# Performance work log

Measured on AMD Instinct MI355X. Metric: run time of the kernel, lower is better.

The kernel has to match this reference:

```python
import jax, jax.numpy as jnp
import numpy as np

B, T, D, H = 4, 2048, 1024, 16
HD = D // H          # head_size = 64
FF = 16 * D          # FeedForward hidden = 16*n_embd per source
EPS = 1e-5


def layer_norm(x, g, b):
    mu = jnp.mean(x, axis=-1, keepdims=True)
    var = jnp.mean(jnp.square(x - mu), axis=-1, keepdims=True)
    return (x - mu) * jax.lax.rsqrt(var + EPS) * g + b


def setup_inputs() -> dict:
    key = jax.random.key(0)
    ks = jax.random.split(key, 17)
    s_d = 1.0 / np.sqrt(D)
    s_ff = 1.0 / np.sqrt(FF)
    return {
        "x": jax.random.normal(ks[0], (B, T, D), jnp.float32),
        # per-head Q/K/V linears, batched over heads: [H, D, HD]
        "Wq": jax.random.normal(ks[1], (H, D, HD), jnp.float32) * s_d,
        "bq": jax.random.normal(ks[2], (H, HD), jnp.float32) * s_d,
        "Wk": jax.random.normal(ks[3], (H, D, HD), jnp.float32) * s_d,
        "bk": jax.random.normal(ks[4], (H, HD), jnp.float32) * s_d,
        "Wv": jax.random.normal(ks[5], (H, D, HD), jnp.float32) * s_d,
        "bv": jax.random.normal(ks[6], (H, HD), jnp.float32) * s_d,
        "Wo": jax.random.normal(ks[7], (D, D), jnp.float32) * s_d,
        "bo": jax.random.normal(ks[8], (D,), jnp.float32) * s_d,
        "ln1_g": jnp.ones((D,), jnp.float32),
        "ln1_b": jnp.zeros((D,), jnp.float32),
        "W1": jax.random.normal(ks[9], (D, FF), jnp.float32) * s_d,
        "b1": jax.random.normal(ks[10], (FF,), jnp.float32) * s_d,
        "W2": jax.random.normal(ks[11], (FF, D), jnp.float32) * s_ff,
        "b2": jax.random.normal(ks[12], (D,), jnp.float32) * s_ff,
        "ln2_g": jnp.ones((D,), jnp.float32),
        "ln2_b": jnp.zeros((D,), jnp.float32),
    }


def reference(x, Wq, bq, Wk, bk, Wv, bv, Wo, bo, ln1_g, ln1_b,
              W1, b1, W2, b2, ln2_g, ln2_b):
    # --- multi-head causal self-attention (all heads batched) ---
    q = jnp.einsum('btd,hdk->bhtk', x, Wq) + bq[None, :, None, :]
    k = jnp.einsum('btd,hdk->bhtk', x, Wk) + bk[None, :, None, :]
    v = jnp.einsum('btd,hdk->bhtk', x, Wv) + bv[None, :, None, :]
    scores = jnp.einsum('bhtk,bhsk->bhts', q, k) / np.sqrt(HD)
    causal = jnp.tril(jnp.ones((T, T), bool))
    scores = jnp.where(causal, scores, -jnp.inf)
    attn = jax.nn.softmax(scores, axis=-1)
    out = jnp.einsum('bhts,bhsk->bhtk', attn, v)
    out = out.transpose(0, 2, 1, 3).reshape(x.shape[0], x.shape[1], H * HD)
    attn_out = out @ Wo + bo
    # --- post-LN residual structure, as in the source ---
    out1 = layer_norm(x + attn_out, ln1_g, ln1_b)
    ff = jax.nn.relu(out1 @ W1 + b1) @ W2 + b2
    out2 = layer_norm(out1 + ff, ln2_g, ln2_b)
    return out2
```

## Files before the change

### kernel.cpp

```cpp
#include <hip/hip_runtime.h>

typedef unsigned short u16;
typedef unsigned int   u32;
typedef __attribute__((ext_vector_type(8))) short short8;
typedef __attribute__((ext_vector_type(4))) float f32x4;

#define DEV static __device__ __forceinline__

DEV u16 f2bf(float x) {
  union { float f; u32 u; } c; c.f = x;
  u32 r = c.u + 0x7fffu + ((c.u >> 16) & 1u);
  return (u16)(r >> 16);
}

struct __align__(8) us4 { u16 a, b, c, d; };

DEV void gload16(const void* g, void* l) {
  __builtin_amdgcn_global_load_lds(
      (const __attribute__((address_space(1))) void*)g,
      (__attribute__((address_space(3))) void*)l, 16, 0, 0);
}

template<int EPI>
__global__ __launch_bounds__(256)
void gemm_bt(const u16* __restrict__ A, const u16* __restrict__ Bt,
             const float* __restrict__ bias, const float* __restrict__ resid,
             float* __restrict__ outf, u16* __restrict__ outb,
             u16* __restrict__ q_out, u16* __restrict__ k_out, u16* __restrict__ vt_out,
             int M, int N, int K)
{
  __shared__ __align__(16) u16 As[128 * 64];
  __shared__ __align__(16) u16 Bs[128 * 64];
  const int tid = threadIdx.x;
  const int lane = tid & 63;
  const int wave = tid >> 6;
  const int wm = wave >> 1, wn = wave & 1;
  const int lo = lane & 15, hi = lane >> 4;

  const int nwg = gridDim.x * gridDim.y;
  int bid = blockIdx.y * gridDim.x + blockIdx.x;
  bid = (bid & 7) * (nwg >> 3) + (bid >> 3);
  const int bm = (bid / gridDim.x) * 128;
  const int bn = (bid % gridDim.x) * 128;

  const int kchunk = K / gridDim.z;
  const int kbeg = blockIdx.z * kchunk;
  const int kend = kbeg + kchunk;

  f32x4 zero = {0.f, 0.f, 0.f, 0.f};
  f32x4 acc[4][4];
#pragma unroll
  for (int i = 0; i < 4; ++i)
#pragma unroll
    for (int j = 0; j < 4; ++j) acc[i][j] = zero;

  for (int k0 = kbeg; k0 < kend; k0 += 64) {
#pragma unroll
    for (int i = 0; i < 4; ++i) {
      int slot = i * 4096 + tid * 16;
      int row  = slot >> 7;
      int c16  = (slot >> 4) & 7;
      int gc   = (c16 ^ (row & 7)) * 8;
      gload16(A  + (size_t)(bm + row) * K + k0 + gc,
              (char*)As + i * 4096 + wave * 1024);
      gload16(Bt + (size_t)(bn + row) * K + k0 + gc,
              (char*)Bs + i * 4096 + wave * 1024);
    }
    __syncthreads();
#pragma unroll
    for (int kk = 0; kk < 2; ++kk) {
      short8 a[4], b[4];
      int ks = kk * 4 + hi;
#pragma unroll
      for (int mi = 0; mi < 4; ++mi) {
        int row = wm * 64 + mi * 16 + lo;
        a[mi] = *(const short8*)&As[row * 64 + ((ks ^ (row & 7)) * 8)];
      }
#pragma unroll
      for (int ni = 0; ni < 4; ++ni) {
        int row = wn * 64 + ni * 16 + lo;
        b[ni] = *(const short8*)&Bs[row * 64 + ((ks ^ (row & 7)) * 8)];
      }
#pragma unroll
      for (int mi = 0; mi < 4; ++mi)
#pragma unroll
        for (int ni = 0; ni < 4; ++ni)
          acc[mi][ni] = __builtin_amdgcn_mfma_f32_16x16x32_bf16(
              a[mi], b[ni], acc[mi][ni], 0, 0, 0);
    }
    __syncthreads();
  }

#pragma unroll
  for (int mi = 0; mi < 4; ++mi) {
#pragma unroll
    for (int ni = 0; ni < 4; ++ni) {
      int col = bn + wn * 64 + ni * 16 + lo;
#pragma unroll
      for (int r = 0; r < 4; ++r) {
        int row = bm + wm * 64 + mi * 16 + hi * 4 + r;
        float v = acc[mi][ni][r];
        if (EPI == 0) {
          v += bias[col];
          int qkv = col >> 10, wc = col & 1023, h = wc >> 6, hd = wc & 63;
          int b_ = row >> 11, t = row & 2047;
          u16 bv = f2bf(v);
          if (qkv == 0)
            q_out[((size_t)((b_ * 16 + h) * 2048 + t)) * 64 + hd] = bv;
          else if (qkv == 1)
            k_out[((size_t)((b_ * 16 + h) * 2048 + t)) * 64 + hd] = bv;
          else
            vt_out[((size_t)((b_ * 16 + h) * 64 + hd)) * 2048 + t] = bv;
        } else if (EPI == 1) {
          v += bias[col] + resid[(size_t)row * N + col];
          outf[(size_t)row * N + col] = v;
        } else if (EPI == 2) {
          v += bias[col];
          v = v > 0.f ? v : 0.f;
          outb[(size_t)row * N + col] = f2bf(v);
        } else {
          atomicAdd(&outf[(size_t)row * N + col], v);
        }
      }
    }
  }
}

__global__ __launch_bounds__(256)
void attn_kernel(const u16* __restrict__ Q, const u16* __restrict__ Kb,
                 const u16* __restrict__ Vt, u16* __restrict__ O)
{
  __shared__ __align__(16) u16 Ks[64 * 64];
  __shared__ __align__(16) u16 Vs[64 * 64];
  __shared__ __align__(16) u16 Pl[4][16 * 80];
  const int tid = threadIdx.x, lane = tid & 63, w = tid >> 6;
  const int lo = lane & 15, hi = lane >> 4;
  const int bh = blockIdx.y;
  const int qt = gridDim.x - 1 - blockIdx.x;
  const int q0 = qt * 64;

  const size_t qbase = ((size_t)bh * 2048 + q0 + w * 16 + lo) * 64;
  short8 qf[2];
  qf[0] = *(const short8*)(Q + qbase + hi * 8);
  qf[1] = *(const short8*)(Q + qbase + 32 + hi * 8);

  float m[4]    = {-1e30f, -1e30f, -1e30f, -1e30f};
  float lsum[4] = {0.f, 0.f, 0.f, 0.f};
  f32x4 zero = {0.f, 0.f, 0.f, 0.f};
  f32x4 oacc[4];
#pragma unroll
  for (int i = 0; i < 4; ++i) oacc[i] = zero;

  const int smax = qt;
  for (int s = 0; s <= smax; ++s) {
#pragma unroll
    for (int i = 0; i < 2; ++i) {
      int slot = i * 4096 + tid * 16;
      int row  = slot >> 7;
      int gc   = (((slot >> 4) & 7) ^ (row & 7)) * 8;
      gload16(Kb + ((size_t)bh * 2048 + s * 64 + row) * 64 + gc,
              (char*)Ks + i * 4096 + w * 1024);
      gload16(Vt + ((size_t)bh * 64 + row) * 2048 + s * 64 + gc,
              (char*)Vs + i * 4096 + w * 1024);
    }
    __syncthreads();

    f32x4 sacc[4];
#pragma unroll
    for (int i = 0; i < 4; ++i) sacc[i] = zero;
#pragma unroll
    for (int ni = 0; ni < 4; ++ni)
#pragma unroll
      for (int kk = 0; kk < 2; ++kk) {
        int row = ni * 16 + lo;
        short8 kf = *(const short8*)&Ks[row * 64 + (((kk * 4 + hi) ^ (row & 7)) * 8)];
        sacc[ni] = __builtin_amdgcn_mfma_f32_16x16x32_bf16(qf[kk], kf, sacc[ni], 0, 0, 0);
      }

    const bool diag = (s == smax);
    float pvv[4][4];
#pragma unroll
    for (int r = 0; r < 4; ++r) {
      int qrow = q0 + w * 16 + hi * 4 + r;
      float mx = -1e30f;
#pragma unroll
      for (int ni = 0; ni < 4; ++ni) {
        float v = sacc[ni][r] * 0.125f;
        int kv = s * 64 + ni * 16 + lo;
        if (diag && kv > qrow) v = -1e30f;
        pvv[ni][r] = v;
        mx = fmaxf(mx, v);
      }
#pragma unroll
      for (int msk = 1; msk < 16; msk <<= 1) mx = fmaxf(mx, __shfl_xor(mx, msk));
      float mnew = fmaxf(m[r], mx);
      float corr = __expf(m[r] - mnew);
      m[r] = mnew;
      float rs = 0.f;
#pragma unroll
      for (int ni = 0; ni < 4; ++ni) {
        float p = __expf(pvv[ni][r] - mnew);
        pvv[ni][r] = p;
        rs += p;
      }
#pragma unroll
      for (int msk = 1; msk < 16; msk <<= 1) rs += __shfl_xor(rs, msk);
      lsum[r] = lsum[r] * corr + rs;
#pragma unroll
      for (int nd = 0; nd < 4; ++nd) oacc[nd][r] *= corr;
    }

#pragma unroll
    for (int ni = 0; ni < 4; ++ni)
#pragma unroll
      for (int r = 0; r < 4; ++r)
        Pl[w][(hi * 4 + r) * 80 + ni * 16 + lo] = f2bf(pvv[ni][r]);

#pragma unroll
    for (int kk = 0; kk < 2; ++kk) {
      short8 pa = *(const short8*)&Pl[w][lo * 80 + kk * 32 + hi * 8];
#pragma unroll
      for (int nd = 0; nd < 4; ++nd) {
        int row = nd * 16 + lo;
        short8 vf = *(const short8*)&Vs[row * 64 + (((kk * 4 + hi) ^ (row & 7)) * 8)];
        oacc[nd] = __builtin_amdgcn_mfma_f32_16x16x32_bf16(pa, vf, oacc[nd], 0, 0, 0);
      }
    }
    __syncthreads();
  }

  const int b_ = bh >> 4, h_ = bh & 15;
#pragma unroll
  for (int r = 0; r < 4; ++r) {
    int t = q0 + w * 16 + hi * 4 + r;
    float inv = 1.f / lsum[r];
    size_t base = ((size_t)b_ * 2048 + t) * 1024 + h_ * 64;
#pragma unroll
    for (int nd = 0; nd < 4; ++nd)
      O[base + nd * 16 + lo] = f2bf(oacc[nd][r] * inv);
  }
}

__global__ __launch_bounds__(256)
void ln_kernel(const float* __restrict__ in, const float* __restrict__ g,
               const float* __restrict__ bp, float* __restrict__ outf,
               u16* __restrict__ outb,
               float* __restrict__ seed_out, const float* __restrict__ seed_bias)
{
  const int row = blockIdx.x, t = threadIdx.x;
  const f32x4 v = *(const f32x4*)(in + (size_t)row * 1024 + t * 4);
  float s  = v[0] + v[1] + v[2] + v[3];
  float sq = v[0] * v[0] + v[1] * v[1] + v[2] * v[2] + v[3] * v[3];
#pragma unroll
  for (int off = 32; off; off >>= 1) {
    s  += __shfl_down(s, off);
    sq += __shfl_down(sq, off);
  }
  __shared__ float red[8];
  const int lane = t & 63, w = t >> 6;
  if (lane == 0) { red[w] = s; red[4 + w] = sq; }
  __syncthreads();
  s  = red[0] + red[1] + red[2] + red[3];
  sq = red[4] + red[5] + red[6] + red[7];
  float mu  = s * (1.f / 1024.f);
  float var = sq * (1.f / 1024.f) - mu * mu;
  float rstd = rsqrtf(var + 1e-5f);
  const f32x4 gv = *(const f32x4*)(g + t * 4);
  const f32x4 bv = *(const f32x4*)(bp + t * 4);
  f32x4 o;
#pragma unroll
  for (int j = 0; j < 4; ++j) o[j] = (v[j] - mu) * rstd * gv[j] + bv[j];
  *(f32x4*)(outf + (size_t)row * 1024 + t * 4) = o;
  if (outb) {
    us4 ob = {f2bf(o[0]), f2bf(o[1]), f2bf(o[2]), f2bf(o[3])};
    *(us4*)(outb + (size_t)row * 1024 + t * 4) = ob;
  }
  if (seed_out) {
    const f32x4 sb = *(const f32x4*)(seed_bias + t * 4);
    f32x4 so = {o[0] + sb[0], o[1] + sb[1], o[2] + sb[2], o[3] + sb[3]};
    *(f32x4*)(seed_out + (size_t)row * 1024 + t * 4) = so;
  }
}

__global__ __launch_bounds__(256)
void cvt_bf16(const float* __restrict__ src, u16* __restrict__ dst, int n4)
{
  int i = blockIdx.x * 256 + threadIdx.x;
  if (i < n4) {
    f32x4 v = *(const f32x4*)(src + (size_t)i * 4);
    us4 o = {f2bf(v[0]), f2bf(v[1]), f2bf(v[2]), f2bf(v[3])};
    *(us4*)(dst + (size_t)i * 4) = o;
  }
}

__global__ __launch_bounds__(256)
void transpose_cvt(const float* __restrict__ src, u16* __restrict__ dst, int R, int C)
{
  __shared__ float tile[64][65];
  const int c0 = blockIdx.x * 64, r0 = blockIdx.y * 64;
  const int t = threadIdx.x;
  const int rl = t >> 4, c4 = (t & 15) * 4;
#pragma unroll
  for (int i = 0; i < 4; ++i) {
    f32x4 v = *(const f32x4*)(src + (size_t)(r0 + rl + i * 16) * C + c0 + c4);
    tile[rl + i * 16][c4 + 0] = v[0];
    tile[rl + i * 16][c4 + 1] = v[1];
    tile[rl + i * 16][c4 + 2] = v[2];
    tile[rl + i * 16][c4 + 3] = v[3];
  }
  __syncthreads();
#pragma unroll
  for (int j = 0; j < 16; ++j) {
    int o = t + j * 256;
    int c = o >> 6, r = o & 63;
    dst[(size_t)(c0 + c) * R + r0 + r] = f2bf(tile[r][c]);
  }
}

__global__ __launch_bounds__(256)
void qkv_pack(const float* __restrict__ Wq, const float* __restrict__ Wk,
              const float* __restrict__ Wv, u16* __restrict__ Wt)
{
  const float* src = blockIdx.z == 0 ? Wq : (blockIdx.z == 1 ? Wk : Wv);
  src += (size_t)blockIdx.y * 1024 * 64;
  __shared__ float tile[64][65];
  const int k0 = blockIdx.x * 64;
  const int t = threadIdx.x;
  const int rl = t >> 4, c4 = (t & 15) * 4;
#pragma unroll
  for (int i = 0; i < 4; ++i) {
    f32x4 v = *(const f32x4*)(src + (size_t)(k0 + rl + i * 16) * 64 + c4);
    tile[rl + i * 16][c4 + 0] = v[0];
    tile[rl + i * 16][c4 + 1] = v[1];
    tile[rl + i * 16][c4 + 2] = v[2];
    tile[rl + i * 16][c4 + 3] = v[3];
  }
  __syncthreads();
  size_t nbase = (size_t)blockIdx.z * 1024 + blockIdx.y * 64;
#pragma unroll
  for (int j = 0; j < 16; ++j) {
    int o = t + j * 256;
    int hd = o >> 6, r = o & 63;
    Wt[(nbase + hd) * 1024 + k0 + r] = f2bf(tile[r][hd]);
  }
}

__global__ void bias_pack(const float* __restrict__ bq, const float* __restrict__ bk,
                          const float* __restrict__ bv, float* __restrict__ out)
{
  int i = blockIdx.x * 256 + threadIdx.x;
  if (i < 3072) {
    const float* s = (i >> 10) == 0 ? bq : ((i >> 10) == 1 ? bk : bv);
    out[i] = s[i & 1023];
  }
}

extern "C" void kernel_launch(void* const* d_in, const int* in_sizes, int n_in,
                              void* d_out, int out_size, void* d_ws, size_t ws_size,
                              hipStream_t stream)
{
  const float* x    = (const float*)d_in[0];
  const float* Wq   = (const float*)d_in[1];
  const float* bq   = (const float*)d_in[2];
  const float* Wk   = (const float*)d_in[3];
  const float* bk   = (const float*)d_in[4];
  const float* Wv   = (const float*)d_in[5];
  const float* bv   = (const float*)d_in[6];
  const float* Wo   = (const float*)d_in[7];
  const float* bo   = (const float*)d_in[8];
  const float* ln1g = (const float*)d_in[9];
  const float* ln1b = (const float*)d_in[10];
  const float* W1   = (const float*)d_in[11];
  const float* b1   = (const float*)d_in[12];
  const float* W2   = (const float*)d_in[13];
  const float* b2   = (const float*)d_in[14];
  const float* ln2g = (const float*)d_in[15];
  const float* ln2b = (const float*)d_in[16];
  float* out = (float*)d_out;

  char* ws = (char*)d_ws;
  const size_t MB = 1ull << 20;
  u16*   Wqkvt = (u16*)(ws + 0);
  float* bqkv  = (float*)(ws + 6 * MB);
  u16*   Wot   = (u16*)(ws + 7 * MB);
  u16*   W1t   = (u16*)(ws + 9 * MB);
  u16*   W2t   = (u16*)(ws + 41 * MB);
  u16*   out1b = (u16*)(ws + 73 * MB);
  float* y1    = (float*)(ws + 89 * MB);
  u16*   Xb    = (u16*)(ws + 121 * MB);
  u16*   Qb    = (u16*)(ws + 137 * MB);
  u16*   Kb    = (u16*)(ws + 153 * MB);
  u16*   Vt    = (u16*)(ws + 169 * MB);
  u16*   attnb = (u16*)(ws + 185 * MB);
  u16*   h_buf = (u16*)(ws + 121 * MB);
  float* y2    = out;

  const int nchunks = (ws_size >= 377 * MB) ? 1 : 4;
  const int Mc      = 8192 / nchunks;
  const int zsplit  = (nchunks == 1) ? 4 : 8;

  cvt_bf16<<<8192, 256, 0, stream>>>(x, Xb, 8192 * 1024 / 4);
  qkv_pack<<<dim3(16, 16, 3), 256, 0, stream>>>(Wq, Wk, Wv, Wqkvt);
  bias_pack<<<12, 256, 0, stream>>>(bq, bk, bv, bqkv);
  transpose_cvt<<<dim3(16, 16), 256, 0, stream>>>(Wo, Wot, 1024, 1024);
  transpose_cvt<<<dim3(256, 16), 256, 0, stream>>>(W1, W1t, 1024, 16384);
  transpose_cvt<<<dim3(16, 256), 256, 0, stream>>>(W2, W2t, 16384, 1024);

  gemm_bt<0><<<dim3(24, 64), 256, 0, stream>>>(Xb, Wqkvt, bqkv, nullptr,
      nullptr, nullptr, Qb, Kb, Vt, 8192, 3072, 1024);

  attn_kernel<<<dim3(32, 64), 256, 0, stream>>>(Qb, Kb, Vt, attnb);

  gemm_bt<1><<<dim3(8, 64), 256, 0, stream>>>(attnb, Wot, bo, x,
      y1, nullptr, nullptr, nullptr, nullptr, 8192, 1024, 1024);

  ln_kernel<<<8192, 256, 0, stream>>>(y1, ln1g, ln1b, y1, out1b, y2, b2);

  for (int c = 0; c < nchunks; ++c) {
    gemm_bt<2><<<dim3(128, Mc / 128), 256, 0, stream>>>(
        out1b + (size_t)c * Mc * 1024, W1t, b1, nullptr,
        nullptr, h_buf, nullptr, nullptr, nullptr, Mc, 16384, 1024);
    gemm_bt<3><<<dim3(8, Mc / 128, zsplit), 256, 0, stream>>>(
        h_buf, W2t, nullptr, nullptr,
        y2 + (size_t)c * Mc * 1024, nullptr, nullptr, nullptr, nullptr,
        Mc, 1024, 16384);
  }

  ln_kernel<<<8192, 256, 0, stream>>>(y2, ln2g, ln2b, out, nullptr,
                                      nullptr, nullptr);

  (void)in_sizes; (void)n_in; (void)out_size;
}
```

Baseline: 1.483 ms.

## Load K/V fragments directly from global memory in attention, drop LDS staging

The attention kernel no longer stages K and V tiles through shared memory with block-wide barriers. Each lane now reads its MFMA operand fragments straight from global memory, relying on the cache for reuse across the four waves. The P scratch buffer gets an XOR swizzle to cut bank conflicts. This removes the two __syncthreads per KV step and the LDS round trip, but the four waves now issue redundant global loads and memory latency is exposed without explicit prefetch.

```diff
diff --git a/kernel.cpp b/kernel.cpp
--- a/kernel.cpp
+++ b/kernel.cpp
@@ -130,8 +130,6 @@
 void attn_kernel(const u16* __restrict__ Q, const u16* __restrict__ Kb,
                  const u16* __restrict__ Vt, u16* __restrict__ O)
 {
-  __shared__ __align__(16) u16 Ks[64 * 64];
-  __shared__ __align__(16) u16 Vs[64 * 64];
   __shared__ __align__(16) u16 Pl[4][16 * 80];
   const int tid = threadIdx.x, lane = tid & 63, w = tid >> 6;
   const int lo = lane & 15, hi = lane >> 4;
@@ -144,6 +142,9 @@
   qf[0] = *(const short8*)(Q + qbase + hi * 8);
   qf[1] = *(const short8*)(Q + qbase + 32 + hi * 8);
 
+  const u16* kbase = Kb + ((size_t)bh * 2048 + lo) * 64 + hi * 8;
+  const u16* vbase = Vt + ((size_t)bh * 64 + lo) * 2048 + hi * 8;
+
   float m[4]    = {-1e30f, -1e30f, -1e30f, -1e30f};
   float lsum[4] = {0.f, 0.f, 0.f, 0.f};
   f32x4 zero = {0.f, 0.f, 0.f, 0.f};
@@ -153,29 +154,18 @@
 
   const int smax = qt;
   for (int s = 0; s <= smax; ++s) {
-#pragma unroll
-    for (int i = 0; i < 2; ++i) {
-      int slot = i * 4096 + tid * 16;
-      int row  = slot >> 7;
-      int gc   = (((slot >> 4) & 7) ^ (row & 7)) * 8;
-      gload16(Kb + ((size_t)bh * 2048 + s * 64 + row) * 64 + gc,
-              (char*)Ks + i * 4096 + w * 1024);
-      gload16(Vt + ((size_t)bh * 64 + row) * 2048 + s * 64 + gc,
-              (char*)Vs + i * 4096 + w * 1024);
-    }
-    __syncthreads();
+    const u16* kp = kbase + (size_t)s * 64 * 64;
 
     f32x4 sacc[4];
 #pragma unroll
     for (int i = 0; i < 4; ++i) sacc[i] = zero;
 #pragma unroll
-    for (int ni = 0; ni < 4; ++ni)
-#pragma unroll
-      for (int kk = 0; kk < 2; ++kk) {
-        int row = ni * 16 + lo;
-        short8 kf = *(const short8*)&Ks[row * 64 + (((kk * 4 + hi) ^ (row & 7)) * 8)];
-        sacc[ni] = __builtin_amdgcn_mfma_f32_16x16x32_bf16(qf[kk], kf, sacc[ni], 0, 0, 0);
-      }
+    for (int ni = 0; ni < 4; ++ni) {
+      short8 kf0 = *(const short8*)(kp + ni * 1024);
+      short8 kf1 = *(const short8*)(kp + ni * 1024 + 32);
+      sacc[ni] = __builtin_amdgcn_mfma_f32_16x16x32_bf16(qf[0], kf0, sacc[ni], 0, 0, 0);
+      sacc[ni] = __builtin_amdgcn_mfma_f32_16x16x32_bf16(qf[1], kf1, sacc[ni], 0, 0, 0);
+    }
 
     const bool diag = (s == smax);
     float pvv[4][4];
@@ -211,22 +201,25 @@
     }
 
 #pragma unroll
-    for (int ni = 0; ni < 4; ++ni)
-#pragma unroll
-      for (int r = 0; r < 4; ++r)
-        Pl[w][(hi * 4 + r) * 80 + ni * 16 + lo] = f2bf(pvv[ni][r]);
+    for (int ni = 0; ni < 4; ++ni) {
+      int chunk = ni * 2 + (lo >> 3);
+      int wi    = lo & 7;
+#pragma unroll
+      for (int r = 0; r < 4; ++r) {
+        int rowp = hi * 4 + r;
+        Pl[w][rowp * 80 + (((chunk ^ (rowp & 7)) << 3) | wi)] = f2bf(pvv[ni][r]);
+      }
+    }
 
 #pragma unroll
     for (int kk = 0; kk < 2; ++kk) {
-      short8 pa = *(const short8*)&Pl[w][lo * 80 + kk * 32 + hi * 8];
+      short8 pa = *(const short8*)&Pl[w][lo * 80 + (((kk * 4 + hi) ^ (lo & 7)) << 3)];
 #pragma unroll
       for (int nd = 0; nd < 4; ++nd) {
-        int row = nd * 16 + lo;
-        short8 vf = *(const short8*)&Vs[row * 64 + (((kk * 4 + hi) ^ (row & 7)) * 8)];
+        short8 vf = *(const short8*)(vbase + (size_t)nd * 16 * 2048 + s * 64 + kk * 32);
         oacc[nd] = __builtin_amdgcn_mfma_f32_16x16x32_bf16(pa, vf, oacc[nd], 0, 0, 0);
       }
     }
-    __syncthreads();
   }
 
   const int b_ = bh >> 4, h_ = bh & 15;
```

Measured after the change: 1.746 ms. 1.18x slower.
